# Optimization experiments

Hardware: AMD Instinct MI355X
Metric: run time of the kernel (lower is better)

## Reference

```python
import jax, jax.numpy as jnp
import numpy as np

HID = 2048
NUM_V, NUM_K = 32, 16
DK, DV = 128, 128
KEY_DIM = NUM_K * DK
VALUE_DIM = NUM_V * DV
CONV_DIM = 2 * KEY_DIM + VALUE_DIM
CONV_K = 4
CHUNK = 64
EPS = 1e-6
B, S = 2, 2048


def setup_inputs():
    key = jax.random.key(0)
    ks = jax.random.split(key, 9)
    w = lambda i, shape, sc=0.02: jax.random.normal(ks[i], shape, jnp.float32) * sc
    return {
        "hidden_states": jax.random.normal(ks[0], (B, S, HID), jnp.float32),
        "W_qkv": w(1, (HID, CONV_DIM)),
        "W_z": w(2, (HID, VALUE_DIM)),
        "W_b": w(3, (HID, NUM_V)),
        "W_a": w(4, (HID, NUM_V)),
        "conv_w": w(5, (CONV_DIM, CONV_K), 0.2),
        "dt_bias": jnp.ones((NUM_V,), jnp.float32),
        "A_log": jnp.log(jax.random.uniform(ks[6], (NUM_V,), jnp.float32, 1e-3, 16.0)),
        "norm_w": jnp.ones((DV,), jnp.float32),
        "W_out": w(7, (VALUE_DIM, HID)),
    }


def _l2norm(x, eps=1e-6):
    return x * jax.lax.rsqrt(jnp.sum(x * x, axis=-1, keepdims=True) + eps)


def _causal_conv_silu(x, w):
    # x: [B, C, S]; depthwise causal conv (kernel K), then SiLU. K is tiny (4).
    K = w.shape[-1]
    xp = jnp.pad(x, ((0, 0), (0, 0), (K - 1, 0)))
    out = sum(xp[:, :, j:j + x.shape[-1]] * w[None, :, j, None] for j in range(K))
    return jax.nn.silu(out)


def _chunk_gated_delta_rule(q, k, v, g, beta, chunk=CHUNK):
    # q,k: [B,S,H,DK]; v: [B,S,H,DV]; g,beta: [B,S,H]. S divisible by chunk.
    q, k = _l2norm(q), _l2norm(k)
    tr = lambda x: jnp.swapaxes(x, 1, 2)
    q, k, v, g, beta = tr(q), tr(k), tr(v), tr(g), tr(beta)  # [B,H,S,...]
    Bb, Hh, Ss, Dk = k.shape
    NC = Ss // chunk
    q = q * (Dk ** -0.5)
    k_beta = k * beta[..., None]
    v_beta = v * beta[..., None]
    ch = lambda x: x.reshape(Bb, Hh, NC, chunk, x.shape[-1])
    q, k, k_beta, v_beta = ch(q), ch(k), ch(k_beta), ch(v_beta)
    g = jnp.cumsum(g.reshape(Bb, Hh, NC, chunk), axis=-1)  # intra-chunk cumulative log-decay
    tril = jnp.tril(jnp.ones((chunk, chunk), bool))
    strict = jnp.tril(jnp.ones((chunk, chunk), bool), -1)
    diff = g[..., :, None] - g[..., None, :]
    dm = jnp.where(tril, jnp.exp(jnp.where(tril, diff, 0.0)), 0.0)  # decay mask, incl. diag
    # strictly-lower A; (I - A) is unit lower triangular -> M = (I - A)^{-1}
    A = -(k_beta @ jnp.swapaxes(k, -1, -2)) * dm * strict
    eye = jnp.eye(chunk, dtype=q.dtype)
    M = jax.scipy.linalg.solve_triangular(eye - A, jnp.broadcast_to(eye, A.shape), lower=True)
    v_c = M @ v_beta
    k_cd = M @ (k_beta * jnp.exp(g)[..., None])

    def step(state, xs):
        q_i, k_i, v_i, g_i, dm_i, kcd_i = xs
        attn_i = (q_i @ jnp.swapaxes(k_i, -1, -2)) * dm_i
        v_new = v_i - kcd_i @ state
        out = (q_i * jnp.exp(g_i)[..., None]) @ state + attn_i @ v_new
        g_last = g_i[..., -1:]
        k_dec = k_i * jnp.exp(g_last - g_i)[..., None]
        state = state * jnp.exp(g_last)[..., None] + jnp.einsum('bhck,bhcv->bhkv', k_dec, v_new)
        return state, out

    mv = lambda x: jnp.moveaxis(x, 2, 0)
    state0 = jnp.zeros((Bb, Hh, Dk, v_c.shape[-1]), q.dtype)
    _, outs = jax.lax.scan(step, state0, (mv(q), mv(k), mv(v_c), mv(g), mv(dm), mv(k_cd)))
    out = jnp.moveaxis(outs, 0, 2).reshape(Bb, Hh, Ss, -1)
    return jnp.swapaxes(out, 1, 2)  # [B,S,H,DV]


def reference(hidden_states, W_qkv, W_z, W_b, W_a, conv_w, dt_bias, A_log, norm_w, W_out):
    Bb, Ss, _ = hidden_states.shape
    mixed = jnp.swapaxes(hidden_states @ W_qkv, 1, 2)  # [B, CONV_DIM, S]
    z = (hidden_states @ W_z).reshape(Bb, Ss, NUM_V, DV)
    beta = jax.nn.sigmoid(hidden_states @ W_b)  # [B,S,NUM_V]
    g = -jnp.exp(A_log) * jax.nn.softplus((hidden_states @ W_a) + dt_bias)
    mixed = _causal_conv_silu(mixed, conv_w)
    mixed = jnp.swapaxes(mixed, 1, 2)  # [B,S,CONV_DIM]
    q = mixed[..., :KEY_DIM].reshape(Bb, Ss, NUM_K, DK)
    k = mixed[..., KEY_DIM:2 * KEY_DIM].reshape(Bb, Ss, NUM_K, DK)
    v = mixed[..., 2 * KEY_DIM:].reshape(Bb, Ss, NUM_V, DV)
    rep = NUM_V // NUM_K
    q = jnp.repeat(q, rep, axis=2)
    k = jnp.repeat(k, rep, axis=2)
    core = _chunk_gated_delta_rule(q, k, v, g, beta)  # [B,S,NUM_V,DV]
    # RMSNormGated: gate with silu(z) before normalization (Mamba2/Qwen3-Next style)
    gated = core * jax.nn.silu(z)
    var = jnp.mean(gated * gated, axis=-1, keepdims=True)
    core = gated * jax.lax.rsqrt(var + EPS) * norm_w
    return core.reshape(Bb, Ss, VALUE_DIM) @ W_out
```

## Files before the change

### kernel.cpp

```cpp
#include <hip/hip_runtime.h>
#include <cstdint>
#include <cstddef>


#define ROWS  4096
#define SEQ   2048
#define HIDN  2048
#define CONVD 8192
#define NWP   12288
#define NUMV  32

using bf16x8 = __attribute__((ext_vector_type(8))) short;
using f32x4v = __attribute__((ext_vector_type(4))) float;

__device__ __forceinline__ float bf2f(unsigned short u) {
  union { unsigned int i; float f; } x; x.i = ((unsigned int)u) << 16; return x.f;
}
__device__ __forceinline__ unsigned short f2bf(float f) {
  union { float f; unsigned int u; } x; x.f = f;
  unsigned int u = x.u;
  unsigned int r = (u + 0x7FFFu + ((u >> 16) & 1u)) >> 16;
  return (unsigned short)r;
}

typedef const __attribute__((address_space(1))) unsigned int GU32;
typedef __attribute__((address_space(3))) unsigned int LU32;
__device__ __forceinline__ void gld_lds16(const void* g, void* l) {
  GU32* gp = (GU32*)(unsigned long long)(uintptr_t)g;
  LU32* lp = (LU32*)(unsigned int)(uintptr_t)l;
  __builtin_amdgcn_global_load_lds(gp, lp, 16, 0, 0);
}
template <int N>
__device__ __forceinline__ void waitcnt_vm() {
  asm volatile("s_waitcnt vmcnt(%0)" ::"i"(N) : "memory");
}

__global__ __launch_bounds__(256) void cast_kernel(const float* __restrict__ in,
                                                   unsigned short* __restrict__ out, int n4) {
  int i = blockIdx.x * 256 + threadIdx.x;
  if (i >= n4) return;
  float4 v = ((const float4*)in)[i];
  ushort4 o;
  o.x = f2bf(v.x); o.y = f2bf(v.y); o.z = f2bf(v.z); o.w = f2bf(v.w);
  ((ushort4*)out)[i] = o;
}

__global__ __launch_bounds__(256) void transpose_kernel(const float* __restrict__ W,
                                                        unsigned short* __restrict__ WT,
                                                        int K, int N, int ld, int roff) {
  __shared__ float tile[64][65];
  const int t = threadIdx.x;
  const int kb = blockIdx.y * 64, nb = blockIdx.x * 64;
  const int r = t >> 2, c0 = (t & 3) * 16;
#pragma unroll
  for (int i = 0; i < 16; ++i) {
    int c = c0 + i;
    float v = 0.f;
    if (nb + c < N) v = W[(size_t)(kb + r) * N + nb + c];
    tile[r][c] = v;
  }
  __syncthreads();
  const int bn = t >> 2, seg = (t & 3) * 16;
  if (nb + bn < N) {
    unsigned short tmp[16];
#pragma unroll
    for (int i = 0; i < 16; ++i) tmp[i] = f2bf(tile[seg + i][bn]);
    unsigned short* dst = WT + (size_t)(roff + nb + bn) * ld + kb + seg;
    *(uint4*)dst = *(const uint4*)&tmp[0];
    *(uint4*)(dst + 8) = *(const uint4*)&tmp[8];
  }
}

__global__ __launch_bounds__(256) void ba_kernel(const unsigned short* __restrict__ hsb,
                                                 const unsigned short* __restrict__ WbaT,
                                                 const float* __restrict__ dt_bias,
                                                 const float* __restrict__ A_log,
                                                 float* __restrict__ G, float* __restrict__ BETA) {
  __shared__ unsigned short hsl[8][2048];
  __shared__ float pacc[4][8][64];
  const int t = threadIdx.x;
  const int lane = t & 63, w = t >> 6;
  const int row0 = blockIdx.x * 8;
#pragma unroll
  for (int rr = 0; rr < 2; ++rr) {
    const int r = w * 2 + rr;
    const unsigned short* src = hsb + (size_t)(row0 + r) * 2048 + lane * 32;
#pragma unroll
    for (int j = 0; j < 8; ++j)
      *(ushort4*)&hsl[r][lane * 32 + j * 4] = *(const ushort4*)(src + j * 4);
  }
  __syncthreads();
  const unsigned short* wrow = WbaT + (size_t)lane * 2048 + w * 512;
  float acc[8] = {0.f, 0.f, 0.f, 0.f, 0.f, 0.f, 0.f, 0.f};
  const int kb0 = w * 512;
#pragma unroll 1
  for (int k = 0; k < 512; k += 4) {
    ushort4 wv = *(const ushort4*)(wrow + k);
    const float w0 = bf2f(wv.x), w1 = bf2f(wv.y), w2 = bf2f(wv.z), w3 = bf2f(wv.w);
#pragma unroll
    for (int r = 0; r < 8; ++r) {
      ushort4 hv = *(const ushort4*)&hsl[r][kb0 + k];
      acc[r] += bf2f(hv.x) * w0 + bf2f(hv.y) * w1 + bf2f(hv.z) * w2 + bf2f(hv.w) * w3;
    }
  }
#pragma unroll
  for (int r = 0; r < 8; ++r) pacc[w][r][lane] = acc[r];
  __syncthreads();
  const int r = t >> 5, hc = t & 31;
  float bp = pacc[0][r][hc] + pacc[1][r][hc] + pacc[2][r][hc] + pacc[3][r][hc];
  float ap = pacc[0][r][32 + hc] + pacc[1][r][32 + hc] + pacc[2][r][32 + hc] + pacc[3][r][32 + hc];
  const int idx = (row0 + r) * NUMV + hc;
  BETA[idx] = 1.f / (1.f + __expf(-bp));
  float x = ap + dt_bias[hc];
  float sp = (x > 15.f) ? x : log1pf(__expf(x));
  G[idx] = -__expf(A_log[hc]) * sp;
}

template <int BM, int BN, int OUT_BF16>
__global__ __launch_bounds__(512) void gemm_r5_kernel(const unsigned short* __restrict__ Ag,
                                                      const unsigned short* __restrict__ Bg,
                                                      void* __restrict__ Cg, int M, int N, int K) {
  constexpr int PM = BM / 2, PN = BN / 4;
  constexpr int MT = PM / 16, NTF = PN / 16;
  constexpr int NA = BM / 128, NB = BN / 128;
  constexpr int LPS = NA + NB;
  constexpr int REG = (BM + BN) * 64;
  extern __shared__ char lds[];
  const int t = threadIdx.x;
  const int lane = t & 63, wid = t >> 6;
  const int wm = wid >> 2, wn = wid & 3;
  const int rlo = lane & 15, khi = lane >> 4;

  const int gx = gridDim.x, nwg = gx * gridDim.y;
  int id = blockIdx.y * gx + blockIdx.x;
  int sid = (id & 7) * (nwg >> 3) + (id >> 3);
  const int m0 = (sid / gx) * BM, n0 = (sid % gx) * BN;

  const int NT = K >> 6;
  const int NPH = NT * 2;

  const int srow = t >> 2;
  const int scs = ((t & 3) * 16) ^ (((t >> 3) & 3) << 4);
  const char* Ap[NA];
  const char* Bp[NB];
#pragma unroll
  for (int i = 0; i < NA; ++i)
    Ap[i] = (const char*)Ag + (size_t)(m0 + i * 128 + srow) * K * 2 + scs;
#pragma unroll
  for (int i = 0; i < NB; ++i)
    Bp[i] = (const char*)Bg + (size_t)(n0 + i * 128 + srow) * K * 2 + scs;
  char* dst = lds + t * 16;

  int offA[MT], offB[NTF];
#pragma unroll
  for (int mi = 0; mi < MT; ++mi) {
    int o = (wm * PM + mi * 16 + rlo) * 64 + khi * 16;
    o ^= ((o >> 7) & 3) << 4;
    offA[mi] = o;
  }
#pragma unroll
  for (int ni = 0; ni < NTF; ++ni) {
    int o = (wn * PN + ni * 16 + rlo) * 64 + khi * 16;
    o ^= ((o >> 7) & 3) << 4;
    offB[ni] = o + BM * 64;
  }

  f32x4v acc[MT][NTF];
#pragma unroll
  for (int mi = 0; mi < MT; ++mi)
#pragma unroll
    for (int ni = 0; ni < NTF; ++ni) acc[mi][ni] = (f32x4v){0.f, 0.f, 0.f, 0.f};

#define STG(PS, R)                                                           \
  do {                                                                       \
    int kts_ = ((PS) >> 1 < NT) ? ((PS) >> 1) : NT - 1;                      \
    size_t co_ = (size_t)kts_ * 128 + (size_t)((PS) & 1) * 64;               \
    char* d_ = dst + (size_t)(R) * REG;                                      \
    _Pragma("unroll") for (int i_ = 0; i_ < NA; ++i_)                        \
        gld_lds16(Ap[i_] + co_, d_ + i_ * 8192);                             \
    _Pragma("unroll") for (int i_ = 0; i_ < NB; ++i_)                        \
        gld_lds16(Bp[i_] + co_, d_ + BM * 64 + i_ * 8192);                   \
  } while (0)

  STG(0, 0); STG(1, 1); STG(2, 2);
  waitcnt_vm<LPS>();
  __builtin_amdgcn_s_barrier();
  __builtin_amdgcn_sched_barrier(0);

  int rA = 0;
#pragma unroll 1
  for (int q = 0; q < NPH / 2; ++q) {
    const int p0 = q * 2;
    int rB = rA + 1; if (rB >= 5) rB -= 5;
    int tA = rA + 3; if (tA >= 5) tA -= 5;
    int tB = rA + 4; if (tB >= 5) tB -= 5;

    {
      const char* rb = lds + (size_t)rA * REG;
      bf16x8 af[MT], bv[NTF];
#pragma unroll
      for (int mi = 0; mi < MT; ++mi) af[mi] = *(const bf16x8*)(rb + offA[mi]);
#pragma unroll
      for (int ni = 0; ni < NTF; ++ni) bv[ni] = *(const bf16x8*)(rb + offB[ni]);
      STG(p0 + 3, tA);
      __builtin_amdgcn_s_setprio(1);
#pragma unroll
      for (int mi = 0; mi < MT; ++mi)
#pragma unroll
        for (int ni = 0; ni < NTF; ++ni)
          acc[mi][ni] = __builtin_amdgcn_mfma_f32_16x16x32_bf16(af[mi], bv[ni], acc[mi][ni], 0, 0, 0);
      __builtin_amdgcn_s_setprio(0);
    }
    {
      const char* rb = lds + (size_t)rB * REG;
      bf16x8 af[MT], bv[NTF];
#pragma unroll
      for (int mi = 0; mi < MT; ++mi) af[mi] = *(const bf16x8*)(rb + offA[mi]);
#pragma unroll
      for (int ni = 0; ni < NTF; ++ni) bv[ni] = *(const bf16x8*)(rb + offB[ni]);
      STG(p0 + 4, tB);
      __builtin_amdgcn_s_setprio(1);
#pragma unroll
      for (int mi = 0; mi < MT; ++mi)
#pragma unroll
        for (int ni = 0; ni < NTF; ++ni)
          acc[mi][ni] = __builtin_amdgcn_mfma_f32_16x16x32_bf16(af[mi], bv[ni], acc[mi][ni], 0, 0, 0);
      __builtin_amdgcn_s_setprio(0);
    }
    waitcnt_vm<LPS>();
    __builtin_amdgcn_s_barrier();
    __builtin_amdgcn_sched_barrier(0);
    rA += 2; if (rA >= 5) rA -= 5;
  }
#undef STG
  waitcnt_vm<0>();

  const int mrb = khi * 4;
#pragma unroll
  for (int mi = 0; mi < MT; ++mi)
#pragma unroll
    for (int ni = 0; ni < NTF; ++ni)
#pragma unroll
      for (int r = 0; r < 4; ++r) {
        int mm = m0 + wm * PM + mi * 16 + mrb + r;
        int nn = n0 + wn * PN + ni * 16 + rlo;
        float v = acc[mi][ni][r];
        if (OUT_BF16) ((unsigned short*)Cg)[(size_t)mm * N + nn] = f2bf(v);
        else          ((float*)Cg)[(size_t)mm * N + nn] = v;
      }
}

__global__ __launch_bounds__(256) void conv_silu_kernel(const unsigned short* __restrict__ C1,
                                                        const float* __restrict__ conv_w,
                                                        unsigned short* __restrict__ QKV) {
  int idx = blockIdx.x * 256 + threadIdx.x;
  int nb = idx >> 11;
  int c4 = (idx & 2047) << 2;
  int row0 = nb * 8;
  int s0 = row0 & 2047;
  float4 w0 = *(const float4*)(conv_w + (size_t)(c4 + 0) * 4);
  float4 w1 = *(const float4*)(conv_w + (size_t)(c4 + 1) * 4);
  float4 w2 = *(const float4*)(conv_w + (size_t)(c4 + 2) * 4);
  float4 w3 = *(const float4*)(conv_w + (size_t)(c4 + 3) * 4);
  const float* pw0 = (const float*)&w0;
  const float* pw1 = (const float*)&w1;
  const float* pw2 = (const float*)&w2;
  const float* pw3 = (const float*)&w3;
  ushort4 rw[11];
#pragma unroll
  for (int i = 0; i < 11; ++i) {
    if (s0 + i >= 3) rw[i] = *(const ushort4*)(C1 + (size_t)(row0 - 3 + i) * NWP + c4);
    else { rw[i].x = 0; rw[i].y = 0; rw[i].z = 0; rw[i].w = 0; }
  }
#pragma unroll
  for (int j = 0; j < 8; ++j) {
    float a0 = 0.f, a1 = 0.f, a2 = 0.f, a3 = 0.f;
#pragma unroll
    for (int jj = 0; jj < 4; ++jj) {
      ushort4 mv = rw[j + jj];
      a0 += bf2f(mv.x) * pw0[jj];
      a1 += bf2f(mv.y) * pw1[jj];
      a2 += bf2f(mv.z) * pw2[jj];
      a3 += bf2f(mv.w) * pw3[jj];
    }
    ushort4 o;
    o.x = f2bf(a0 / (1.f + __expf(-a0)));
    o.y = f2bf(a1 / (1.f + __expf(-a1)));
    o.z = f2bf(a2 / (1.f + __expf(-a2)));
    o.w = f2bf(a3 / (1.f + __expf(-a3)));
    *(ushort4*)(QKV + (size_t)(row0 + j) * CONVD + c4) = o;
  }
}

#define INTRA_SMEM 70144
__global__ __launch_bounds__(256) void intra_kernel(const unsigned short* __restrict__ QKV,
                                                    const float* __restrict__ G,
                                                    const float* __restrict__ BETA,
                                                    unsigned short* __restrict__ WU,
                                                    unsigned short* __restrict__ ATTN) {
  extern __shared__ char smem[];
  unsigned short* ktb = (unsigned short*)smem;
  float* Amat = (float*)(smem + 17408);
  float* Xt   = (float*)(smem + 34816);
  unsigned short* qb = (unsigned short*)Xt;
  float* gc  = (float*)(smem + 69632);
  float* bet = gc + 64;

  const int t = threadIdx.x;
  const int lane = t & 63, w = t >> 6;
  const int rlo = lane & 15, khi = lane >> 4;
  const int cix = blockIdx.x & 31;
  const int h = (blockIdx.x >> 5) & 31;
  const int b = blockIdx.x >> 10;
  const int hq = h >> 1;
  const int row0 = cix * 64;
  const size_t rowbase = (size_t)b * SEQ;

  if (t < 64) {
    float gv = G[(rowbase + row0 + t) * NUMV + h];
    bet[t] = BETA[(rowbase + row0 + t) * NUMV + h];
#pragma unroll
    for (int off = 1; off < 64; off <<= 1) {
      float u = __shfl_up(gv, off, 64);
      if (t >= off) gv += u;
    }
    gc[t] = gv;
  }
  __syncthreads();

  const int r = t >> 2, q4 = t & 3;
  const size_t grow = (rowbase + row0 + r) * (size_t)CONVD;

  {
    const unsigned short* kp = QKV + grow + 2048 + hq * 128 + q4 * 32;
    float kv[32]; float ssk = 0.f;
#pragma unroll
    for (int j = 0; j < 32; j += 4) {
      ushort4 km = *(const ushort4*)(kp + j);
      kv[j] = bf2f(km.x); kv[j + 1] = bf2f(km.y); kv[j + 2] = bf2f(km.z); kv[j + 3] = bf2f(km.w);
      ssk += kv[j]*kv[j] + kv[j+1]*kv[j+1] + kv[j+2]*kv[j+2] + kv[j+3]*kv[j+3];
    }
    ssk += __shfl_xor(ssk, 1, 64);
    ssk += __shfl_xor(ssk, 2, 64);
    const float rk = rsqrtf(ssk + 1e-6f);
    const float ekr = __expf(gc[r]) * bet[r];
#pragma unroll
    for (int j = 0; j < 32; ++j) {
      float kn = kv[j] * rk;
      ktb[r * 136 + q4 * 32 + j] = f2bf(kn);
      Xt[(q4 * 32 + j) * 68 + r] = kn * ekr;
    }
  }
  __syncthreads();

  float xr[64];

  {
    static const signed char SJ[10][2] = {{0,0},{1,0},{1,1},{2,0},{2,1},{2,2},{3,0},{3,1},{3,2},{3,3}};
    static const signed char SB[5] = {0, 3, 6, 8, 10};
    for (int sj = SB[w]; sj < SB[w + 1]; ++sj) {
      const int mt = SJ[sj][0], nt = SJ[sj][1];
      f32x4v acc = (f32x4v){0.f, 0.f, 0.f, 0.f};
#pragma unroll
      for (int ks = 0; ks < 4; ++ks) {
        bf16x8 af = *(const bf16x8*)&ktb[(mt * 16 + rlo) * 136 + ks * 32 + khi * 8];
        bf16x8 bf_ = *(const bf16x8*)&ktb[(nt * 16 + rlo) * 136 + ks * 32 + khi * 8];
        acc = __builtin_amdgcn_mfma_f32_16x16x32_bf16(af, bf_, acc, 0, 0, 0);
      }
      const int j = nt * 16 + rlo;
#pragma unroll
      for (int r2 = 0; r2 < 4; ++r2) {
        const int i = mt * 16 + khi * 4 + r2;
        if (j < i) Amat[i * 68 + j] = -bet[i] * __expf(gc[i] - gc[j]) * acc[r2];
      }
    }
    if (t < 128) {
      const float* Xc = Xt + t * 68;
#pragma unroll
      for (int j = 0; j < 64; j += 4) {
        f32x4v xv = *(const f32x4v*)(Xc + j);
        xr[j] = xv[0]; xr[j + 1] = xv[1]; xr[j + 2] = xv[2]; xr[j + 3] = xv[3];
      }
    }
  }
  __syncthreads();

  {
    const unsigned short* vp = QKV + grow + 4096 + h * 128 + q4 * 32;
    const float brow = bet[r];
#pragma unroll
    for (int j = 0; j < 32; j += 4) {
      ushort4 vm = *(const ushort4*)(vp + j);
      Xt[(q4 * 32 + j + 0) * 68 + r] = bf2f(vm.x) * brow;
      Xt[(q4 * 32 + j + 1) * 68 + r] = bf2f(vm.y) * brow;
      Xt[(q4 * 32 + j + 2) * 68 + r] = bf2f(vm.z) * brow;
      Xt[(q4 * 32 + j + 3) * 68 + r] = bf2f(vm.w) * brow;
    }
  }
  __syncthreads();
  if (t >= 128) {
    const float* Xc = Xt + (t - 128) * 68;
#pragma unroll
    for (int j = 0; j < 64; j += 4) {
      f32x4v xv = *(const f32x4v*)(Xc + j);
      xr[j] = xv[0]; xr[j + 1] = xv[1]; xr[j + 2] = xv[2]; xr[j + 3] = xv[3];
    }
  }
  __syncthreads();

#pragma unroll
  for (int ib = 0; ib < 8; ++ib) {
    const int i0 = ib * 8;
    float p[8] = {0, 0, 0, 0, 0, 0, 0, 0};
#pragma unroll
    for (int j = 0; j < i0; j += 4) {
#pragma unroll
      for (int r2 = 0; r2 < 8; ++r2) {
        f32x4v ar = *(const f32x4v*)&Amat[(i0 + r2) * 68 + j];
        p[r2] += ar[0] * xr[j] + ar[1] * xr[j + 1] + ar[2] * xr[j + 2] + ar[3] * xr[j + 3];
      }
    }
#pragma unroll
    for (int r2 = 0; r2 < 8; ++r2) {
      float v = xr[i0 + r2] + p[r2];
#pragma unroll
      for (int r3 = 0; r3 < r2; ++r3) v += Amat[(i0 + r2) * 68 + i0 + r3] * xr[i0 + r3];
      xr[i0 + r2] = v;
    }
  }

  if (t < 128) {
    float* Xc = Xt + t * 68;
#pragma unroll
    for (int j = 0; j < 64; j += 4) {
      f32x4v xv = {xr[j], xr[j + 1], xr[j + 2], xr[j + 3]};
      *(f32x4v*)(Xc + j) = xv;
    }
  }
  __syncthreads();
  {
    unsigned short* wdst = WU + (rowbase + row0 + r) * (size_t)NWP + h * 128 + q4 * 32;
#pragma unroll
    for (int j = 0; j < 32; ++j) wdst[j] = f2bf(Xt[(q4 * 32 + j) * 68 + r]);
  }
  __syncthreads();
  if (t >= 128) {
    float* Xc = Xt + (t - 128) * 68;
#pragma unroll
    for (int j = 0; j < 64; j += 4) {
      f32x4v xv = {xr[j], xr[j + 1], xr[j + 2], xr[j + 3]};
      *(f32x4v*)(Xc + j) = xv;
    }
  }
  __syncthreads();
  {
    unsigned short* udst = WU + (rowbase + row0 + r) * (size_t)NWP + 4096 + h * 128 + q4 * 32;
#pragma unroll
    for (int j = 0; j < 32; ++j) udst[j] = f2bf(Xt[(q4 * 32 + j) * 68 + r]);
  }
  __syncthreads();

  {
    const unsigned short* qp = QKV + grow + hq * 128 + q4 * 32;
    float qv[32]; float ssq = 0.f;
#pragma unroll
    for (int j = 0; j < 32; j += 4) {
      ushort4 qm = *(const ushort4*)(qp + j);
      qv[j] = bf2f(qm.x); qv[j + 1] = bf2f(qm.y); qv[j + 2] = bf2f(qm.z); qv[j + 3] = bf2f(qm.w);
      ssq += qv[j]*qv[j] + qv[j+1]*qv[j+1] + qv[j+2]*qv[j+2] + qv[j+3]*qv[j+3];
    }
    ssq += __shfl_xor(ssq, 1, 64);
    ssq += __shfl_xor(ssq, 2, 64);
    const float rq = rsqrtf(ssq + 1e-6f) * 0.08838834764831845f;
#pragma unroll
    for (int j = 0; j < 32; ++j) qb[r * 136 + q4 * 32 + j] = f2bf(qv[j] * rq);
  }
  __syncthreads();

  {
    const size_t abase = (((size_t)b * 32 + h) * 32 + cix) * 4096;
    static const signed char CJ[10][2] = {{0,0},{1,0},{1,1},{2,0},{2,1},{2,2},{3,0},{3,1},{3,2},{3,3}};
    static const signed char CB[5] = {0, 3, 6, 8, 10};
    static const signed char ZJ[6][2] = {{0,1},{0,2},{0,3},{1,2},{1,3},{2,3}};
    static const signed char ZB[5] = {0, 0, 0, 3, 6};
#pragma unroll 1
    for (int cj = CB[w]; cj < CB[w + 1]; ++cj) {
      const int bi = CJ[cj][0], nt = CJ[cj][1];
      const int j = nt * 16 + rlo;
      f32x4v acc = (f32x4v){0.f, 0.f, 0.f, 0.f};
#pragma unroll
      for (int ks = 0; ks < 4; ++ks) {
        bf16x8 af = *(const bf16x8*)&qb[(bi * 16 + rlo) * 136 + ks * 32 + khi * 8];
        bf16x8 bf_ = *(const bf16x8*)&ktb[(nt * 16 + rlo) * 136 + ks * 32 + khi * 8];
        acc = __builtin_amdgcn_mfma_f32_16x16x32_bf16(af, bf_, acc, 0, 0, 0);
      }
#pragma unroll
      for (int r2 = 0; r2 < 4; ++r2) {
        const int i = bi * 16 + khi * 4 + r2;
        float v = (j <= i) ? __expf(gc[i] - gc[j]) * acc[r2] : 0.f;
        ATTN[abase + i * 64 + j] = f2bf(v);
      }
    }
#pragma unroll 1
    for (int zj = ZB[w]; zj < ZB[w + 1]; ++zj) {
      const int bi = ZJ[zj][0], nt = ZJ[zj][1];
#pragma unroll
      for (int r2 = 0; r2 < 4; ++r2)
        ATTN[abase + (bi * 16 + khi * 4 + r2) * 64 + nt * 16 + rlo] = 0;
    }
  }
}

#define SEQ_SMEM 70400
__global__ __launch_bounds__(256) void seq_kernel(const unsigned short* __restrict__ QKV,
                                                  const float* __restrict__ G,
                                                  const unsigned short* __restrict__ WU,
                                                  const unsigned short* __restrict__ ATTN,
                                                  unsigned short* __restrict__ CORE) {
  extern __shared__ char smem[];
  unsigned short* ktT    = (unsigned short*)smem;
  unsigned short* wb     = (unsigned short*)(smem + 22528);
  unsigned short* attnb  = (unsigned short*)(smem + 39936);
  float* stateT          = (float*)(smem + 51200);
  unsigned short* stateTb = (unsigned short*)(smem + 59904);
  unsigned short* vnTb   = (unsigned short*)(smem + 64256);
  unsigned short* vdTb   = (unsigned short*)(smem + 67072);

  const int t = threadIdx.x;
  const int lane = t & 63, w = t >> 6;
  const int rlo = lane & 15, khi = lane >> 4;
  const int vq = blockIdx.x & 7;
  const int h = (blockIdx.x >> 3) & 31;
  const int b = blockIdx.x >> 8;
  const int hq = h >> 1;
  const size_t rowbase = (size_t)b * SEQ;
  const size_t ahead = ((size_t)b * 32 + h) * 32;

  for (int i = t; i < 16 * 136; i += 256) { stateT[i] = 0.f; stateTb[i] = 0; }
  __syncthreads();

  bf16x8 qf[4];

#pragma unroll 1
  for (int ncb = 0; ncb < 32; ++ncb) {
    const int row0 = ncb * 64;

    float gv = G[(rowbase + row0 + lane) * NUMV + h];
#pragma unroll
    for (int off = 1; off < 64; off <<= 1) {
      float uph = __shfl_up(gv, off, 64);
      if (lane >= off) gv += uph;
    }
    const float gtot = __shfl(gv, 63, 64);

    {
      const int r = t >> 2, q4 = t & 3;
      const size_t grow = (rowbase + row0 + r) * (size_t)CONVD;
      const unsigned short* kp = QKV + grow + 2048 + hq * 128 + q4 * 32;
      float kv[32]; float ssk = 0.f;
#pragma unroll
      for (int j = 0; j < 32; j += 4) {
        ushort4 km = *(const ushort4*)(kp + j);
        kv[j] = bf2f(km.x); kv[j + 1] = bf2f(km.y); kv[j + 2] = bf2f(km.z); kv[j + 3] = bf2f(km.w);
        ssk += kv[j]*kv[j] + kv[j+1]*kv[j+1] + kv[j+2]*kv[j+2] + kv[j+3]*kv[j+3];
      }
      ssk += __shfl_xor(ssk, 1, 64);
      ssk += __shfl_xor(ssk, 2, 64);
      const float rk = rsqrtf(ssk + 1e-6f);
#pragma unroll
      for (int j = 0; j < 32; ++j) ktT[(q4 * 32 + j) * 88 + r] = f2bf(kv[j] * rk);
      const unsigned short* wsrc = WU + (rowbase + row0 + r) * (size_t)NWP + h * 128 + q4 * 32;
#pragma unroll
      for (int u2 = 0; u2 < 4; ++u2)
        *(uint4*)&wb[r * 136 + q4 * 32 + u2 * 8] = *(const uint4*)(wsrc + u2 * 8);
      const unsigned short* asrc = ATTN + (ahead + ncb) * 4096 + r * 64 + q4 * 16;
      *(uint4*)&attnb[r * 88 + q4 * 16] = *(const uint4*)(asrc);
      *(uint4*)&attnb[r * 88 + q4 * 16 + 8] = *(const uint4*)(asrc + 8);
      const unsigned short* qsrc = QKV + (rowbase + row0 + w * 16 + rlo) * (size_t)CONVD + hq * 128 + khi * 8;
      float qv[32]; float ssq = 0.f;
#pragma unroll
      for (int ks = 0; ks < 4; ++ks) {
        ushort4 qa = *(const ushort4*)(qsrc + ks * 32);
        ushort4 qb2 = *(const ushort4*)(qsrc + ks * 32 + 4);
        qv[ks*8+0] = bf2f(qa.x); qv[ks*8+1] = bf2f(qa.y); qv[ks*8+2] = bf2f(qa.z); qv[ks*8+3] = bf2f(qa.w);
        qv[ks*8+4] = bf2f(qb2.x); qv[ks*8+5] = bf2f(qb2.y); qv[ks*8+6] = bf2f(qb2.z); qv[ks*8+7] = bf2f(qb2.w);
#pragma unroll
        for (int e = 0; e < 8; ++e) ssq += qv[ks*8+e] * qv[ks*8+e];
      }
      ssq += __shfl_xor(ssq, 16, 64);
      ssq += __shfl_xor(ssq, 32, 64);
      const float rq = rsqrtf(ssq + 1e-6f) * 0.08838834764831845f;
#pragma unroll
      for (int ks = 0; ks < 4; ++ks) {
        bf16x8 tv;
#pragma unroll
        for (int e = 0; e < 8; ++e) tv[e] = (short)f2bf(qv[ks*8+e] * rq);
        qf[ks] = tv;
      }
    }
    __syncthreads();

    f32x4v oacc;
    {
      f32x4v pacc = (f32x4v){0.f, 0.f, 0.f, 0.f};
      oacc = (f32x4v){0.f, 0.f, 0.f, 0.f};
#pragma unroll
      for (int ks = 0; ks < 4; ++ks) {
        bf16x8 aw = *(const bf16x8*)&wb[(w * 16 + rlo) * 136 + ks * 32 + khi * 8];
        bf16x8 bs = *(const bf16x8*)&stateTb[rlo * 136 + ks * 32 + khi * 8];
        pacc = __builtin_amdgcn_mfma_f32_16x16x32_bf16(aw, bs, pacc, 0, 0, 0);
        oacc = __builtin_amdgcn_mfma_f32_16x16x32_bf16(qf[ks], bs, oacc, 0, 0, 0);
      }
#pragma unroll
      for (int r2 = 0; r2 < 4; ++r2) {
        const int i = w * 16 + khi * 4 + r2;
        const float gci = __shfl(gv, i, 64);
        float uv = bf2f(WU[(rowbase + row0 + i) * (size_t)NWP + 4096 + h * 128 + vq * 16 + rlo]);
        float vn = uv - pacc[r2];
        vnTb[rlo * 88 + i] = f2bf(vn);
        vdTb[rlo * 88 + i] = f2bf(vn * __expf(gtot - gci));
        oacc[r2] *= __expf(gci);
      }
    }
    __syncthreads();

    {
#pragma unroll
      for (int ks = 0; ks < 2; ++ks) {
        bf16x8 aa = *(const bf16x8*)&attnb[(w * 16 + rlo) * 88 + ks * 32 + khi * 8];
        bf16x8 bv = *(const bf16x8*)&vnTb[rlo * 88 + ks * 32 + khi * 8];
        oacc = __builtin_amdgcn_mfma_f32_16x16x32_bf16(aa, bv, oacc, 0, 0, 0);
      }
      const int col = h * 128 + vq * 16 + rlo;
#pragma unroll
      for (int r2 = 0; r2 < 4; ++r2) {
        const int i = w * 16 + khi * 4 + r2;
        CORE[(rowbase + row0 + i) * (size_t)4096 + col] = f2bf(oacc[r2]);
      }
      const float egl = __expf(gtot);
#pragma unroll
      for (int n2 = 0; n2 < 2; ++n2) {
        const int dt = w * 2 + n2;
        f32x4v sacc = (f32x4v){0.f, 0.f, 0.f, 0.f};
#pragma unroll
        for (int ks = 0; ks < 2; ++ks) {
          bf16x8 ak = *(const bf16x8*)&ktT[(dt * 16 + rlo) * 88 + ks * 32 + khi * 8];
          bf16x8 bv2 = *(const bf16x8*)&vdTb[rlo * 88 + ks * 32 + khi * 8];
          sacc = __builtin_amdgcn_mfma_f32_16x16x32_bf16(ak, bv2, sacc, 0, 0, 0);
        }
#pragma unroll
        for (int r2 = 0; r2 < 4; ++r2) {
          const int d = dt * 16 + khi * 4 + r2;
          float ns = stateT[rlo * 136 + d] * egl + sacc[r2];
          stateT[rlo * 136 + d] = ns;
          stateTb[rlo * 136 + d] = f2bf(ns);
        }
      }
    }
    __syncthreads();
  }
}

__global__ __launch_bounds__(256) void gatenorm_kernel(const unsigned short* __restrict__ CORE,
                                                       const unsigned short* __restrict__ C1,
                                                       const float* __restrict__ norm_w,
                                                       unsigned short* __restrict__ NRM) {
  const int wid = blockIdx.x * 4 + (threadIdx.x >> 6);
  const int lane = threadIdx.x & 63;
  const int row = wid >> 5, h = wid & 31;
  const int c = lane * 2;
  const size_t cidx = (size_t)row * 4096 + h * 128 + c;
  const size_t zidx = (size_t)row * NWP + 8192 + h * 128 + c;
  float g0 = bf2f(CORE[cidx]), g1 = bf2f(CORE[cidx + 1]);
  float z0 = bf2f(C1[zidx]), z1 = bf2f(C1[zidx + 1]);
  g0 *= z0 / (1.f + __expf(-z0));
  g1 *= z1 / (1.f + __expf(-z1));
  float ss = g0 * g0 + g1 * g1;
#pragma unroll
  for (int m = 1; m < 64; m <<= 1) ss += __shfl_xor(ss, m, 64);
  const float rr = rsqrtf(ss * (1.f / 128.f) + 1e-6f);
  unsigned int o = ((unsigned int)f2bf(g1 * rr * norm_w[c + 1]) << 16) | (unsigned int)f2bf(g0 * rr * norm_w[c]);
  *(unsigned int*)(NRM + cidx) = o;
}

extern "C" void kernel_launch(void* const* d_in, const int* in_sizes, int n_in,
                              void* d_out, int out_size, void* d_ws, size_t ws_size,
                              hipStream_t stream) {
  const float* hs      = (const float*)d_in[0];
  const float* W_qkv   = (const float*)d_in[1];
  const float* W_z     = (const float*)d_in[2];
  const float* W_b     = (const float*)d_in[3];
  const float* W_a     = (const float*)d_in[4];
  const float* conv_w  = (const float*)d_in[5];
  const float* dt_bias = (const float*)d_in[6];
  const float* A_log   = (const float*)d_in[7];
  const float* norm_w  = (const float*)d_in[8];
  const float* W_out   = (const float*)d_in[9];
  float* out = (float*)d_out;
  char* ws = (char*)d_ws;

  const size_t OFF_HSB = 0;
  const size_t OFF_WT  = OFF_HSB + (size_t)ROWS * HIDN * 2;
  const size_t OFF_WOT = OFF_WT + (size_t)NWP * HIDN * 2;
  const size_t OFF_WBA = OFF_WOT + (size_t)HIDN * 4096 * 2;
  const size_t OFF_C1  = OFF_WBA + (size_t)64 * HIDN * 2;
  const size_t OFF_QKV = OFF_C1 + (size_t)ROWS * NWP * 2;
  const size_t OFF_G   = OFF_QKV + (size_t)ROWS * CONVD * 2;
  const size_t OFF_B   = OFF_G + (size_t)ROWS * NUMV * 4;

  unsigned short* hsb = (unsigned short*)(ws + OFF_HSB);
  unsigned short* WT  = (unsigned short*)(ws + OFF_WT);
  unsigned short* WoT = (unsigned short*)(ws + OFF_WOT);
  unsigned short* Wba = (unsigned short*)(ws + OFF_WBA);
  unsigned short* C1  = (unsigned short*)(ws + OFF_C1);
  unsigned short* QKV = (unsigned short*)(ws + OFF_QKV);
  float* Gb = (float*)(ws + OFF_G);
  float* Bb = (float*)(ws + OFF_B);
  unsigned short* ATTNb = (unsigned short*)(ws + OFF_HSB);
  unsigned short* COREb = (unsigned short*)(ws + OFF_WT);
  unsigned short* NRMb  = (unsigned short*)(ws + OFF_QKV);

  cast_kernel<<<ROWS * HIDN / 4 / 256, 256, 0, stream>>>(hs, hsb, ROWS * HIDN / 4);
  transpose_kernel<<<dim3(8192 / 64, 2048 / 64), 256, 0, stream>>>(W_qkv, WT, 2048, 8192, HIDN, 0);
  transpose_kernel<<<dim3(4096 / 64, 2048 / 64), 256, 0, stream>>>(W_z, WT, 2048, 4096, HIDN, 8192);
  transpose_kernel<<<dim3(1, 2048 / 64), 256, 0, stream>>>(W_b, Wba, 2048, 32, HIDN, 0);
  transpose_kernel<<<dim3(1, 2048 / 64), 256, 0, stream>>>(W_a, Wba, 2048, 32, HIDN, 32);
  transpose_kernel<<<dim3(2048 / 64, 4096 / 64), 256, 0, stream>>>(W_out, WoT, 4096, 2048, 4096, 0);

  ba_kernel<<<ROWS / 8, 256, 0, stream>>>(hsb, Wba, dt_bias, A_log, Gb, Bb);

  void (*g1p)(const unsigned short*, const unsigned short*, void*, int, int, int) = gemm_r5_kernel<256, 256, 1>;
  void (*g0p)(const unsigned short*, const unsigned short*, void*, int, int, int) = gemm_r5_kernel<128, 256, 0>;
  hipFuncSetAttribute((const void*)g1p, hipFuncAttributeMaxDynamicSharedMemorySize, 5 * (256 + 256) * 64);
  hipFuncSetAttribute((const void*)g0p, hipFuncAttributeMaxDynamicSharedMemorySize, 5 * (128 + 256) * 64);

  gemm_r5_kernel<256, 256, 1><<<dim3(NWP / 256, ROWS / 256), 512, 5 * (256 + 256) * 64, stream>>>(
      hsb, WT, C1, ROWS, NWP, HIDN);
  conv_silu_kernel<<<(ROWS / 8) * 2048 / 256, 256, 0, stream>>>(C1, conv_w, QKV);

  hipFuncSetAttribute((const void*)intra_kernel, hipFuncAttributeMaxDynamicSharedMemorySize,
                      INTRA_SMEM);
  intra_kernel<<<2048, 256, INTRA_SMEM, stream>>>(QKV, Gb, Bb, C1, ATTNb);

  hipFuncSetAttribute((const void*)seq_kernel, hipFuncAttributeMaxDynamicSharedMemorySize,
                      SEQ_SMEM);
  seq_kernel<<<512, 256, SEQ_SMEM, stream>>>(QKV, Gb, C1, ATTNb, COREb);

  gatenorm_kernel<<<ROWS * NUMV / 4, 256, 0, stream>>>(COREb, C1, norm_w, NRMb);
  gemm_r5_kernel<128, 256, 0><<<dim3(2048 / 256, ROWS / 128), 512, 5 * (128 + 256) * 64, stream>>>(
      NRMb, WoT, out, ROWS, 2048, 4096);
}
```

Before: 755.0 us.

## Pad leading dimensions of all workspace buffers to break power-of-two strides

Every intermediate buffer (bf16 hidden states, transposed weights, the QKV/Z projection output, the conv output and the core output) now uses a padded row stride instead of an exact power of two. The GEMM kernel gains explicit lda/ldb/ldc arguments, and the cast, conv, intra, seq and gatenorm kernels index with the new strides. The aim is to reduce memory-channel and cache-set conflicts caused by many rows mapping to the same addresses under power-of-two strides. In exchange the workspace grows slightly and every address calculation across the kernels must stay consistent with the new strides.

```diff
diff --git a/kernel.cpp b/kernel.cpp
--- a/kernel.cpp
+++ b/kernel.cpp
@@ -6,9 +6,15 @@
 #define ROWS  4096
 #define SEQ   2048
 #define HIDN  2048
-#define CONVD 8192
 #define NWP   12288
 #define NUMV  32
+
+#define LDH   2080
+#define LDW   2080
+#define LDWO  4160
+#define LDC1  12416
+#define LDQ   8256
+#define LDCO  4160
 
 using bf16x8 = __attribute__((ext_vector_type(8))) short;
 using f32x4v = __attribute__((ext_vector_type(4))) float;
@@ -36,13 +42,16 @@
 }
 
 __global__ __launch_bounds__(256) void cast_kernel(const float* __restrict__ in,
-                                                   unsigned short* __restrict__ out, int n4) {
+                                                   unsigned short* __restrict__ out) {
   int i = blockIdx.x * 256 + threadIdx.x;
-  if (i >= n4) return;
-  float4 v = ((const float4*)in)[i];
-  ushort4 o;
-  o.x = f2bf(v.x); o.y = f2bf(v.y); o.z = f2bf(v.z); o.w = f2bf(v.w);
-  ((ushort4*)out)[i] = o;
+  int row = i >> 8;
+  int c8 = (i & 255) * 8;
+  float4 v0 = *(const float4*)(in + (size_t)row * 2048 + c8);
+  float4 v1 = *(const float4*)(in + (size_t)row * 2048 + c8 + 4);
+  unsigned short o[8];
+  o[0] = f2bf(v0.x); o[1] = f2bf(v0.y); o[2] = f2bf(v0.z); o[3] = f2bf(v0.w);
+  o[4] = f2bf(v1.x); o[5] = f2bf(v1.y); o[6] = f2bf(v1.z); o[7] = f2bf(v1.w);
+  *(uint4*)(out + (size_t)row * LDH + c8) = *(const uint4*)o;
 }
 
 __global__ __launch_bounds__(256) void transpose_kernel(const float* __restrict__ W,
@@ -84,13 +93,13 @@
 #pragma unroll
   for (int rr = 0; rr < 2; ++rr) {
     const int r = w * 2 + rr;
-    const unsigned short* src = hsb + (size_t)(row0 + r) * 2048 + lane * 32;
+    const unsigned short* src = hsb + (size_t)(row0 + r) * LDH + lane * 32;
 #pragma unroll
     for (int j = 0; j < 8; ++j)
       *(ushort4*)&hsl[r][lane * 32 + j * 4] = *(const ushort4*)(src + j * 4);
   }
   __syncthreads();
-  const unsigned short* wrow = WbaT + (size_t)lane * 2048 + w * 512;
+  const unsigned short* wrow = WbaT + (size_t)lane * LDW + w * 512;
   float acc[8] = {0.f, 0.f, 0.f, 0.f, 0.f, 0.f, 0.f, 0.f};
   const int kb0 = w * 512;
 #pragma unroll 1
@@ -119,7 +128,8 @@
 template <int BM, int BN, int OUT_BF16>
 __global__ __launch_bounds__(512) void gemm_r5_kernel(const unsigned short* __restrict__ Ag,
                                                       const unsigned short* __restrict__ Bg,
-                                                      void* __restrict__ Cg, int M, int N, int K) {
+                                                      void* __restrict__ Cg, int M, int N, int K,
+                                                      int lda, int ldb, int ldc) {
   constexpr int PM = BM / 2, PN = BN / 4;
   constexpr int MT = PM / 16, NTF = PN / 16;
   constexpr int NA = BM / 128, NB = BN / 128;
@@ -145,10 +155,10 @@
   const char* Bp[NB];
 #pragma unroll
   for (int i = 0; i < NA; ++i)
-    Ap[i] = (const char*)Ag + (size_t)(m0 + i * 128 + srow) * K * 2 + scs;
+    Ap[i] = (const char*)Ag + (size_t)(m0 + i * 128 + srow) * lda * 2 + scs;
 #pragma unroll
   for (int i = 0; i < NB; ++i)
-    Bp[i] = (const char*)Bg + (size_t)(n0 + i * 128 + srow) * K * 2 + scs;
+    Bp[i] = (const char*)Bg + (size_t)(n0 + i * 128 + srow) * ldb * 2 + scs;
   char* dst = lds + t * 16;
 
   int offA[MT], offB[NTF];
@@ -245,8 +255,8 @@
         int mm = m0 + wm * PM + mi * 16 + mrb + r;
         int nn = n0 + wn * PN + ni * 16 + rlo;
         float v = acc[mi][ni][r];
-        if (OUT_BF16) ((unsigned short*)Cg)[(size_t)mm * N + nn] = f2bf(v);
-        else          ((float*)Cg)[(size_t)mm * N + nn] = v;
+        if (OUT_BF16) ((unsigned short*)Cg)[(size_t)mm * ldc + nn] = f2bf(v);
+        else          ((float*)Cg)[(size_t)mm * ldc + nn] = v;
       }
 }
 
@@ -269,7 +279,7 @@
   ushort4 rw[11];
 #pragma unroll
   for (int i = 0; i < 11; ++i) {
-    if (s0 + i >= 3) rw[i] = *(const ushort4*)(C1 + (size_t)(row0 - 3 + i) * NWP + c4);
+    if (s0 + i >= 3) rw[i] = *(const ushort4*)(C1 + (size_t)(row0 - 3 + i) * LDC1 + c4);
     else { rw[i].x = 0; rw[i].y = 0; rw[i].z = 0; rw[i].w = 0; }
   }
 #pragma unroll
@@ -288,7 +298,7 @@
     o.y = f2bf(a1 / (1.f + __expf(-a1)));
     o.z = f2bf(a2 / (1.f + __expf(-a2)));
     o.w = f2bf(a3 / (1.f + __expf(-a3)));
-    *(ushort4*)(QKV + (size_t)(row0 + j) * CONVD + c4) = o;
+    *(ushort4*)(QKV + (size_t)(row0 + j) * LDQ + c4) = o;
   }
 }
 
@@ -329,7 +339,7 @@
   __syncthreads();
 
   const int r = t >> 2, q4 = t & 3;
-  const size_t grow = (rowbase + row0 + r) * (size_t)CONVD;
+  const size_t grow = (rowbase + row0 + r) * (size_t)LDQ;
 
   {
     const unsigned short* kp = QKV + grow + 2048 + hq * 128 + q4 * 32;
@@ -439,7 +449,7 @@
   }
   __syncthreads();
   {
-    unsigned short* wdst = WU + (rowbase + row0 + r) * (size_t)NWP + h * 128 + q4 * 32;
+    unsigned short* wdst = WU + (rowbase + row0 + r) * (size_t)LDC1 + h * 128 + q4 * 32;
 #pragma unroll
     for (int j = 0; j < 32; ++j) wdst[j] = f2bf(Xt[(q4 * 32 + j) * 68 + r]);
   }
@@ -454,7 +464,7 @@
   }
   __syncthreads();
   {
-    unsigned short* udst = WU + (rowbase + row0 + r) * (size_t)NWP + 4096 + h * 128 + q4 * 32;
+    unsigned short* udst = WU + (rowbase + row0 + r) * (size_t)LDC1 + 4096 + h * 128 + q4 * 32;
 #pragma unroll
     for (int j = 0; j < 32; ++j) udst[j] = f2bf(Xt[(q4 * 32 + j) * 68 + r]);
   }
@@ -555,7 +565,7 @@
 
     {
       const int r = t >> 2, q4 = t & 3;
-      const size_t grow = (rowbase + row0 + r) * (size_t)CONVD;
+      const size_t grow = (rowbase + row0 + r) * (size_t)LDQ;
       const unsigned short* kp = QKV + grow + 2048 + hq * 128 + q4 * 32;
       float kv[32]; float ssk = 0.f;
 #pragma unroll
@@ -569,14 +579,14 @@
       const float rk = rsqrtf(ssk + 1e-6f);
 #pragma unroll
       for (int j = 0; j < 32; ++j) ktT[(q4 * 32 + j) * 88 + r] = f2bf(kv[j] * rk);
-      const unsigned short* wsrc = WU + (rowbase + row0 + r) * (size_t)NWP + h * 128 + q4 * 32;
+      const unsigned short* wsrc = WU + (rowbase + row0 + r) * (size_t)LDC1 + h * 128 + q4 * 32;
 #pragma unroll
       for (int u2 = 0; u2 < 4; ++u2)
         *(uint4*)&wb[r * 136 + q4 * 32 + u2 * 8] = *(const uint4*)(wsrc + u2 * 8);
       const unsigned short* asrc = ATTN + (ahead + ncb) * 4096 + r * 64 + q4 * 16;
       *(uint4*)&attnb[r * 88 + q4 * 16] = *(const uint4*)(asrc);
       *(uint4*)&attnb[r * 88 + q4 * 16 + 8] = *(const uint4*)(asrc + 8);
-      const unsigned short* qsrc = QKV + (rowbase + row0 + w * 16 + rlo) * (size_t)CONVD + hq * 128 + khi * 8;
+      const unsigned short* qsrc = QKV + (rowbase + row0 + w * 16 + rlo) * (size_t)LDQ + hq * 128 + khi * 8;
       float qv[32]; float ssq = 0.f;
 #pragma unroll
       for (int ks = 0; ks < 4; ++ks) {
@@ -615,7 +625,7 @@
       for (int r2 = 0; r2 < 4; ++r2) {
         const int i = w * 16 + khi * 4 + r2;
         const float gci = __shfl(gv, i, 64);
-        float uv = bf2f(WU[(rowbase + row0 + i) * (size_t)NWP + 4096 + h * 128 + vq * 16 + rlo]);
+        float uv = bf2f(WU[(rowbase + row0 + i) * (size_t)LDC1 + 4096 + h * 128 + vq * 16 + rlo]);
         float vn = uv - pacc[r2];
         vnTb[rlo * 88 + i] = f2bf(vn);
         vdTb[rlo * 88 + i] = f2bf(vn * __expf(gtot - gci));
@@ -635,7 +645,7 @@
 #pragma unroll
       for (int r2 = 0; r2 < 4; ++r2) {
         const int i = w * 16 + khi * 4 + r2;
-        CORE[(rowbase + row0 + i) * (size_t)4096 + col] = f2bf(oacc[r2]);
+        CORE[(rowbase + row0 + i) * (size_t)LDCO + col] = f2bf(oacc[r2]);
       }
       const float egl = __expf(gtot);
 #pragma unroll
@@ -669,8 +679,8 @@
   const int lane = threadIdx.x & 63;
   const int row = wid >> 5, h = wid & 31;
   const int c = lane * 2;
-  const size_t cidx = (size_t)row * 4096 + h * 128 + c;
-  const size_t zidx = (size_t)row * NWP + 8192 + h * 128 + c;
+  const size_t cidx = (size_t)row * LDCO + h * 128 + c;
+  const size_t zidx = (size_t)row * LDC1 + 8192 + h * 128 + c;
   float g0 = bf2f(CORE[cidx]), g1 = bf2f(CORE[cidx + 1]);
   float z0 = bf2f(C1[zidx]), z1 = bf2f(C1[zidx + 1]);
   g0 *= z0 / (1.f + __expf(-z0));
@@ -700,12 +710,12 @@
   char* ws = (char*)d_ws;
 
   const size_t OFF_HSB = 0;
-  const size_t OFF_WT  = OFF_HSB + (size_t)ROWS * HIDN * 2;
-  const size_t OFF_WOT = OFF_WT + (size_t)NWP * HIDN * 2;
-  const size_t OFF_WBA = OFF_WOT + (size_t)HIDN * 4096 * 2;
-  const size_t OFF_C1  = OFF_WBA + (size_t)64 * HIDN * 2;
-  const size_t OFF_QKV = OFF_C1 + (size_t)ROWS * NWP * 2;
-  const size_t OFF_G   = OFF_QKV + (size_t)ROWS * CONVD * 2;
+  const size_t OFF_WT  = OFF_HSB + (size_t)ROWS * LDH * 2;
+  const size_t OFF_WOT = OFF_WT + (size_t)NWP * LDW * 2;
+  const size_t OFF_WBA = OFF_WOT + (size_t)HIDN * LDWO * 2;
+  const size_t OFF_C1  = OFF_WBA + (size_t)64 * LDW * 2;
+  const size_t OFF_QKV = OFF_C1 + (size_t)ROWS * LDC1 * 2;
+  const size_t OFF_G   = OFF_QKV + (size_t)ROWS * LDQ * 2;
   const size_t OFF_B   = OFF_G + (size_t)ROWS * NUMV * 4;
 
   unsigned short* hsb = (unsigned short*)(ws + OFF_HSB);
@@ -720,22 +730,24 @@
   unsigned short* COREb = (unsigned short*)(ws + OFF_WT);
   unsigned short* NRMb  = (unsigned short*)(ws + OFF_QKV);
 
-  cast_kernel<<<ROWS * HIDN / 4 / 256, 256, 0, stream>>>(hs, hsb, ROWS * HIDN / 4);
-  transpose_kernel<<<dim3(8192 / 64, 2048 / 64), 256, 0, stream>>>(W_qkv, WT, 2048, 8192, HIDN, 0);
-  transpose_kernel<<<dim3(4096 / 64, 2048 / 64), 256, 0, stream>>>(W_z, WT, 2048, 4096, HIDN, 8192);
-  transpose_kernel<<<dim3(1, 2048 / 64), 256, 0, stream>>>(W_b, Wba, 2048, 32, HIDN, 0);
-  transpose_kernel<<<dim3(1, 2048 / 64), 256, 0, stream>>>(W_a, Wba, 2048, 32, HIDN, 32);
-  transpose_kernel<<<dim3(2048 / 64, 4096 / 64), 256, 0, stream>>>(W_out, WoT, 4096, 2048, 4096, 0);
+  cast_kernel<<<ROWS, 256, 0, stream>>>(hs, hsb);
+  transpose_kernel<<<dim3(8192 / 64, 2048 / 64), 256, 0, stream>>>(W_qkv, WT, 2048, 8192, LDW, 0);
+  transpose_kernel<<<dim3(4096 / 64, 2048 / 64), 256, 0, stream>>>(W_z, WT, 2048, 4096, LDW, 8192);
+  transpose_kernel<<<dim3(1, 2048 / 64), 256, 0, stream>>>(W_b, Wba, 2048, 32, LDW, 0);
+  transpose_kernel<<<dim3(1, 2048 / 64), 256, 0, stream>>>(W_a, Wba, 2048, 32, LDW, 32);
+  transpose_kernel<<<dim3(2048 / 64, 4096 / 64), 256, 0, stream>>>(W_out, WoT, 4096, 2048, LDWO, 0);
 
   ba_kernel<<<ROWS / 8, 256, 0, stream>>>(hsb, Wba, dt_bias, A_log, Gb, Bb);
 
-  void (*g1p)(const unsigned short*, const unsigned short*, void*, int, int, int) = gemm_r5_kernel<256, 256, 1>;
-  void (*g0p)(const unsigned short*, const unsigned short*, void*, int, int, int) = gemm_r5_kernel<128, 256, 0>;
+  void (*g1p)(const unsigned short*, const unsigned short*, void*, int, int, int, int, int, int) =
+      gemm_r5_kernel<256, 256, 1>;
+  void (*g0p)(const unsigned short*, const unsigned short*, void*, int, int, int, int, int, int) =
+      gemm_r5_kernel<128, 256, 0>;
   hipFuncSetAttribute((const void*)g1p, hipFuncAttributeMaxDynamicSharedMemorySize, 5 * (256 + 256) * 64);
   hipFuncSetAttribute((const void*)g0p, hipFuncAttributeMaxDynamicSharedMemorySize, 5 * (128 + 256) * 64);
 
   gemm_r5_kernel<256, 256, 1><<<dim3(NWP / 256, ROWS / 256), 512, 5 * (256 + 256) * 64, stream>>>(
-      hsb, WT, C1, ROWS, NWP, HIDN);
+      hsb, WT, C1, ROWS, NWP, HIDN, LDH, LDW, LDC1);
   conv_silu_kernel<<<(ROWS / 8) * 2048 / 256, 256, 0, stream>>>(C1, conv_w, QKV);
 
   hipFuncSetAttribute((const void*)intra_kernel, hipFuncAttributeMaxDynamicSharedMemorySize,
@@ -748,5 +760,5 @@
 
   gatenorm_kernel<<<ROWS * NUMV / 4, 256, 0, stream>>>(COREb, C1, norm_w, NRMb);
   gemm_r5_kernel<128, 256, 0><<<dim3(2048 / 256, ROWS / 128), 512, 5 * (128 + 256) * 64, stream>>>(
-      NRMb, WoT, out, ROWS, 2048, 4096);
-}
+      NRMb, WoT, out, ROWS, 2048, 4096, LDCO, LDWO, 2048);
+}
```

Measured after the change: 754.9 us. About the same (-0.0%).
